# Performance work log

Hardware: AMD Instinct MI355X
Metric: run time of the kernel (lower is better)

## Reference

```python
import jax, jax.numpy as jnp
import numpy as np

D = 1024
H = 16
DH = D // H


def setup_inputs() -> dict:
    key = jax.random.key(0)
    ks = jax.random.split(key, 9)
    s = 1.0 / np.sqrt(D)
    x = jax.random.normal(ks[0], (4, 2048, D), dtype=jnp.float32)
    Wq = jax.random.uniform(ks[1], (D, D), jnp.float32, -s, s)
    bq = jax.random.uniform(ks[2], (D,), jnp.float32, -s, s)
    Wk = jax.random.uniform(ks[3], (D, D), jnp.float32, -s, s)
    bk = jax.random.uniform(ks[4], (D,), jnp.float32, -s, s)
    Wv = jax.random.uniform(ks[5], (D, D), jnp.float32, -s, s)
    bv = jax.random.uniform(ks[6], (D,), jnp.float32, -s, s)
    Wo = jax.random.uniform(ks[7], (D, D), jnp.float32, -s, s)
    bo = jax.random.uniform(ks[8], (D,), jnp.float32, -s, s)
    return {"x": x, "Wq": Wq, "bq": bq, "Wk": Wk, "bk": bk,
            "Wv": Wv, "bv": bv, "Wo": Wo, "bo": bo}


def _split_heads(t):
    b, s, d = t.shape
    return t.reshape(b, s, H, DH).transpose(0, 2, 1, 3)  # (B,H,S,Dh)


def reference(x, Wq, bq, Wk, bk, Wv, bv, Wo, bo):
    # Self-attention: context = x
    q = _split_heads(x @ Wq.T + bq)
    k = _split_heads(x @ Wk.T + bk)
    v = _split_heads(x @ Wv.T + bv)
    scale = 1.0 / np.sqrt(DH).astype(np.float32)
    logits = jnp.einsum('bhqd,bhkd->bhqk', q, k) * scale
    attn = jax.nn.softmax(logits, axis=-1)
    out_h = jnp.einsum('bhqk,bhkd->bhqd', attn, v)  # (B,H,S,Dh)
    b, h, s, dh = out_h.shape
    out = out_h.transpose(0, 2, 1, 3).reshape(b, s, h * dh)
    return out @ Wo.T + bo
```

## Files before the change

kernel.cpp:

```cpp
#include <hip/hip_runtime.h>
#include <cstdint>
#include <cstddef>

typedef unsigned short u16;
typedef __attribute__((ext_vector_type(8))) short short8;
typedef __attribute__((ext_vector_type(4))) short sv4;
typedef __attribute__((ext_vector_type(4))) float f32x4;
typedef __attribute__((ext_vector_type(2))) unsigned int u32x2;
typedef __attribute__((ext_vector_type(4))) unsigned int u32x4;

__device__ __forceinline__ u16 f2bf(float f) {
  unsigned int u = __builtin_bit_cast(unsigned int, f);
  u += 0x7FFFu + ((u >> 16) & 1u);
  return (u16)(u >> 16);
}
__device__ __forceinline__ float bf2f(u16 v) {
  return __builtin_bit_cast(float, ((unsigned int)v) << 16);
}

__device__ __forceinline__ unsigned int pk_bf16(float a, float b) {
#if defined(__HIP_DEVICE_COMPILE__) && __has_builtin(__builtin_amdgcn_cvt_pk_bf16_f32)
  typedef __attribute__((ext_vector_type(2))) __bf16 bf16x2;
  bf16x2 r = __builtin_amdgcn_cvt_pk_bf16_f32(a, b);
  return __builtin_bit_cast(unsigned int, r);
#else
  return (unsigned int)f2bf(a) | ((unsigned int)f2bf(b) << 16);
#endif
}

__device__ __forceinline__ f32x4 mfma_16x16x16_bf16(sv4 a, sv4 b, f32x4 c) {
#if defined(__HIP_DEVICE_COMPILE__)
#if __has_builtin(__builtin_amdgcn_mfma_f32_16x16x16bf16_1k)
  return __builtin_amdgcn_mfma_f32_16x16x16bf16_1k(a, b, c, 0, 0, 0);
#elif __has_builtin(__builtin_amdgcn_mfma_f32_16x16x16_bf16)
  return __builtin_amdgcn_mfma_f32_16x16x16_bf16(a, b, c, 0, 0, 0);
#else
  asm volatile("v_mfma_f32_16x16x16_bf16 %0, %1, %2, %0\n\ts_nop 7\n\ts_nop 4"
               : "+v"(c) : "v"(a), "v"(b));
  return c;
#endif
#else
  (void)a; (void)b;
  return c;
#endif
}

#define GLD_LDS(g, l) __builtin_amdgcn_global_load_lds( \
    (const __attribute__((address_space(1))) void*)(g), \
    (__attribute__((address_space(3))) void*)(l), 16, 0, 0)

#define QSCL 0.18033688011112042f

__global__ void detect_dtype(const u16* __restrict__ x, int* __restrict__ flag)
{
  const int lane = threadIdx.x;
  int hit = 0;
#pragma unroll
  for (int j = 0; j < 4; ++j) {
    float v = bf2f(x[lane * 4 + j]);
    if (!(v > -1000.f && v < 1000.f)) hit = 1;
  }
  unsigned long long any = __ballot(hit != 0);
  if (lane == 0) *flag = (any != 0ull) ? 1 : 0;
}

__global__ __launch_bounds__(256)
void convert_wb(const void* Wq, const void* Wk, const void* Wv, const void* Wo,
                const void* bq, const void* bk, const void* bv, const void* bo,
                u16* __restrict__ Wc, u16* __restrict__ bc, const int* __restrict__ flag)
{
  const int fp32 = *flag;
  const size_t base = ((size_t)blockIdx.x * 256 + threadIdx.x) * 8;
  const void* src; u16* dst; size_t local; int sel;
  if (base < (size_t)4 * 1048576) {
    sel = (int)(base >> 20);
    local = base & 1048575u;
    src = (sel == 0) ? Wq : (sel == 1) ? Wk : (sel == 2) ? Wv : Wo;
    dst = Wc + (size_t)sel * 1048576 + local;
  } else {
    const size_t rem = base - (size_t)4 * 1048576;
    sel = (int)(rem >> 10);
    local = rem & 1023u;
    src = (sel == 0) ? bq : (sel == 1) ? bk : (sel == 2) ? bv : bo;
    dst = bc + (size_t)sel * 1024 + local;
  }
  const float scale = (sel == 0) ? QSCL : 1.0f;
  if (fp32) {
    const float* s = (const float*)src + local;
    u32x4 w;
#pragma unroll
    for (int j = 0; j < 4; ++j) w[j] = pk_bf16(s[2 * j] * scale, s[2 * j + 1] * scale);
    *(short8*)dst = __builtin_bit_cast(short8, w);
  } else {
    const u16* s = (const u16*)src + local;
    if (sel == 0) {
      u32x4 w;
#pragma unroll
      for (int j = 0; j < 4; ++j)
        w[j] = pk_bf16(bf2f(s[2 * j]) * scale, bf2f(s[2 * j + 1]) * scale);
      *(short8*)dst = __builtin_bit_cast(short8, w);
    } else {
      *(short8*)dst = *(const short8*)s;
    }
  }
}

__global__ __launch_bounds__(256)
void convert_x_off(const void* __restrict__ x, u16* __restrict__ dst,
                   const int* __restrict__ flag, int b)
{
  const int fp32 = *flag;
  const size_t base = ((size_t)blockIdx.x * 256 + threadIdx.x) * 8;
  const size_t src_e = (size_t)b * 2048 * 1024 + base;
  if (fp32) {
    const float* s = (const float*)x + src_e;
    u32x4 w;
#pragma unroll
    for (int j = 0; j < 4; ++j) w[j] = pk_bf16(s[2 * j], s[2 * j + 1]);
    *(short8*)(dst + base) = __builtin_bit_cast(short8, w);
  } else {
    *(short8*)(dst + base) = *(const short8*)((const u16*)x + src_e);
  }
}

__global__ __launch_bounds__(256)
void gemm_bt(const u16* __restrict__ A,
             const u16* __restrict__ B0, const u16* __restrict__ B1, const u16* __restrict__ B2,
             const u16* __restrict__ bias, u16* __restrict__ C, int Ntot, int K)
{
  __shared__ __align__(16) u16 Alds[128 * 32];
  __shared__ __align__(16) u16 Blds[128 * 32];
  const int tid  = threadIdx.x;
  const int wave = tid >> 6, lane = tid & 63;
  const int quad = lane >> 4, l15 = lane & 15;
  const int m0  = blockIdx.x * 128;
  const int n0g = blockIdx.y * 128;
  const int sel = n0g >> 10;
  const u16* Bm = (sel == 0) ? B0 : ((sel == 1) ? B1 : B2);
  const u16* bb = bias + (size_t)sel * 1024;
  const int n0 = n0g & 1023;
  const int wr = (wave >> 1) * 64, wc = (wave & 1) * 64;

  f32x4 acc[4][4] = {};
  const int srow = lane >> 2;
  const int skc  = (lane & 3) * 8;
  const u16* Ag = A  + (size_t)(m0 + srow) * K + skc;
  const u16* Bg = Bm + (size_t)(n0 + srow) * K + skc;

  for (int kt = 0; kt < K; kt += 32) {
    __syncthreads();
#pragma unroll
    for (int t = 0; t < 2; ++t) {
      const int seg = wave * 2 + t;
      GLD_LDS(Ag + (size_t)(seg * 16) * K + kt, Alds + seg * 512);
      GLD_LDS(Bg + (size_t)(seg * 16) * K + kt, Blds + seg * 512);
    }
    __syncthreads();

    short8 af[4], bfr[4];
#pragma unroll
    for (int i = 0; i < 4; ++i)
      af[i] = *(const short8*)&Alds[(wr + i * 16 + l15) * 32 + quad * 8];
#pragma unroll
    for (int j = 0; j < 4; ++j)
      bfr[j] = *(const short8*)&Blds[(wc + j * 16 + l15) * 32 + quad * 8];
#pragma unroll
    for (int i = 0; i < 4; ++i)
#pragma unroll
      for (int j = 0; j < 4; ++j)
        acc[i][j] = __builtin_amdgcn_mfma_f32_16x16x32_bf16(af[i], bfr[j], acc[i][j], 0, 0, 0);
  }

#pragma unroll
  for (int i = 0; i < 4; ++i) {
    const int mr = m0 + wr + i * 16 + quad * 4;
#pragma unroll
    for (int j = 0; j < 4; ++j) {
      const int ncl = wc + j * 16 + l15;
      const float bvv = bf2f(bb[n0 + ncl]);
#pragma unroll
      for (int r = 0; r < 4; ++r)
        C[(size_t)(mr + r) * Ntot + n0g + ncl] = f2bf(acc[i][j][r] + bvv);
    }
  }
}

__global__ __launch_bounds__(256)
void gemm_bt_out(const u16* __restrict__ A, const u16* __restrict__ Bm,
                 const u16* __restrict__ bias, void* __restrict__ C16,
                 void* __restrict__ C32, int Ntot, int K, const int* __restrict__ flag)
{
  __shared__ __align__(16) u16 Alds[128 * 32];
  __shared__ __align__(16) u16 Blds[128 * 32];
  const int tid  = threadIdx.x;
  const int wave = tid >> 6, lane = tid & 63;
  const int quad = lane >> 4, l15 = lane & 15;
  const int m0 = blockIdx.x * 128;
  const int n0 = blockIdx.y * 128;
  const int wr = (wave >> 1) * 64, wc = (wave & 1) * 64;

  f32x4 acc[4][4] = {};
  const int srow = lane >> 2;
  const int skc  = (lane & 3) * 8;
  const u16* Ag = A  + (size_t)(m0 + srow) * K + skc;
  const u16* Bg = Bm + (size_t)(n0 + srow) * K + skc;

  for (int kt = 0; kt < K; kt += 32) {
    __syncthreads();
#pragma unroll
    for (int t = 0; t < 2; ++t) {
      const int seg = wave * 2 + t;
      GLD_LDS(Ag + (size_t)(seg * 16) * K + kt, Alds + seg * 512);
      GLD_LDS(Bg + (size_t)(seg * 16) * K + kt, Blds + seg * 512);
    }
    __syncthreads();

    short8 af[4], bfr[4];
#pragma unroll
    for (int i = 0; i < 4; ++i)
      af[i] = *(const short8*)&Alds[(wr + i * 16 + l15) * 32 + quad * 8];
#pragma unroll
    for (int j = 0; j < 4; ++j)
      bfr[j] = *(const short8*)&Blds[(wc + j * 16 + l15) * 32 + quad * 8];
#pragma unroll
    for (int i = 0; i < 4; ++i)
#pragma unroll
      for (int j = 0; j < 4; ++j)
        acc[i][j] = __builtin_amdgcn_mfma_f32_16x16x32_bf16(af[i], bfr[j], acc[i][j], 0, 0, 0);
  }

  if (*flag != 0) {
    float* Cf = (float*)C32;
#pragma unroll
    for (int i = 0; i < 4; ++i) {
      const int mr = m0 + wr + i * 16 + quad * 4;
#pragma unroll
      for (int j = 0; j < 4; ++j) {
        const int ncl = wc + j * 16 + l15;
        const float bvv = bf2f(bias[n0 + ncl]);
#pragma unroll
        for (int r = 0; r < 4; ++r)
          Cf[(size_t)(mr + r) * Ntot + n0 + ncl] = acc[i][j][r] + bvv;
      }
    }
  } else {
    u16* Cb = (u16*)C16;
#pragma unroll
    for (int i = 0; i < 4; ++i) {
      const int mr = m0 + wr + i * 16 + quad * 4;
#pragma unroll
      for (int j = 0; j < 4; ++j) {
        const int ncl = wc + j * 16 + l15;
        const float bvv = bf2f(bias[n0 + ncl]);
#pragma unroll
        for (int r = 0; r < 4; ++r)
          Cb[(size_t)(mr + r) * Ntot + n0 + ncl] = f2bf(acc[i][j][r] + bvv);
      }
    }
  }
}

__global__ __launch_bounds__(256, 4)
void attn_s(const u16* __restrict__ QKV, u16* __restrict__ O)
{
  __shared__ __align__(16) u16 Klds[64 * 72];
  __shared__ __align__(16) unsigned int Vlds[64 * 32];
  const int tid  = threadIdx.x;
  const int wave = tid >> 6, lane = tid & 63;
  const int quad = lane >> 4, l15 = lane & 15;
  const int qt = blockIdx.x, h = blockIdx.y;
  const u16* QKVb = QKV + (size_t)blockIdx.z * 2048 * 3072;
  u16* Ob = O + (size_t)blockIdx.z * 2048 * 1024;
  const int q0 = qt * 128;

  short8 qf[2][2];
  const u16* Qb = QKVb + (size_t)(q0 + wave * 32) * 3072 + h * 64;
#pragma unroll
  for (int rt = 0; rt < 2; ++rt)
#pragma unroll
    for (int kh = 0; kh < 2; ++kh)
      qf[rt][kh] = *(const short8*)(Qb + (size_t)(rt * 16 + l15) * 3072 + kh * 32 + quad * 8);

  f32x4 oaccT[4][2] = {};
  float lrow[2] = {};

  const int ksrow = tid >> 2;
  const int kscb  = (tid & 3) * 16;
  const int vkvp = lane & 31;
  const int vd0  = wave * 16 + (lane >> 5) * 8;

  const u16* Kb = QKVb + 1024 + h * 64;
  const u16* Vb = QKVb + 2048 + h * 64;

  for (int kv0 = 0; kv0 < 2048; kv0 += 64) {
    __syncthreads();
    {
      const u16* kp = Kb + (size_t)(kv0 + ksrow) * 3072 + kscb;
      *(short8*)&Klds[ksrow * 72 + kscb]     = *(const short8*)kp;
      *(short8*)&Klds[ksrow * 72 + kscb + 8] = *(const short8*)(kp + 8);

      const u16* v0p = Vb + (size_t)(kv0 + 2 * vkvp) * 3072 + vd0;
      short8 va = *(const short8*)v0p;
      short8 vb2 = *(const short8*)(v0p + 3072);
      const int kb = vkvp >> 1, kl = vkvp & 1;
#pragma unroll
      for (int j = 0; j < 8; ++j) {
        const int d = vd0 + j;
        Vlds[d * 32 + ((kb ^ (d & 15)) << 1) + kl] =
            ((unsigned int)(unsigned short)va[j]) |
            (((unsigned int)(unsigned short)vb2[j]) << 16);
      }
    }
    __syncthreads();

    f32x4 sacc[4][2] = {};
#pragma unroll
    for (int kh = 0; kh < 2; ++kh) {
      short8 kf[4];
#pragma unroll
      for (int ct = 0; ct < 4; ++ct)
        kf[ct] = *(const short8*)&Klds[(ct * 16 + l15) * 72 + kh * 32 + quad * 8];
#pragma unroll
      for (int ct = 0; ct < 4; ++ct)
#pragma unroll
        for (int rt = 0; rt < 2; ++rt)
          sacc[ct][rt] = __builtin_amdgcn_mfma_f32_16x16x32_bf16(kf[ct], qf[rt][kh], sacc[ct][rt], 0, 0, 0);
    }

    sv4 p16[4][2];
#pragma unroll
    for (int rt = 0; rt < 2; ++rt) {
      float rs = 0.f;
#pragma unroll
      for (int ct = 0; ct < 4; ++ct) {
        float p0 = __builtin_amdgcn_exp2f(sacc[ct][rt][0]);
        float p1 = __builtin_amdgcn_exp2f(sacc[ct][rt][1]);
        float p2 = __builtin_amdgcn_exp2f(sacc[ct][rt][2]);
        float p3 = __builtin_amdgcn_exp2f(sacc[ct][rt][3]);
        rs += (p0 + p1) + (p2 + p3);
        u32x2 pw;
        pw[0] = pk_bf16(p0, p1);
        pw[1] = pk_bf16(p2, p3);
        p16[ct][rt] = __builtin_bit_cast(sv4, pw);
      }
      rs += __shfl_xor(rs, 16, 64);
      rs += __shfl_xor(rs, 32, 64);
      lrow[rt] += rs;
    }

#pragma unroll
    for (int ct = 0; ct < 4; ++ct) {
#pragma unroll
      for (int dt = 0; dt < 4; ++dt) {
        const int d = dt * 16 + l15;
        const int idx = d * 32 + (((ct * 4 + quad) ^ (d & 15)) << 1);
        const sv4 vfr = *(const sv4*)&Vlds[idx];
#pragma unroll
        for (int rt = 0; rt < 2; ++rt)
          oaccT[dt][rt] = mfma_16x16x16_bf16(vfr, p16[ct][rt], oaccT[dt][rt]);
      }
    }
  }

#pragma unroll
  for (int rt = 0; rt < 2; ++rt) {
    const float inv = 1.f / lrow[rt];
    u16* Op = Ob + (size_t)(q0 + wave * 32 + rt * 16 + l15) * 1024 + h * 64;
#pragma unroll
    for (int dt = 0; dt < 4; ++dt) {
      u32x2 ow;
      ow[0] = pk_bf16(oaccT[dt][rt][0] * inv, oaccT[dt][rt][1] * inv);
      ow[1] = pk_bf16(oaccT[dt][rt][2] * inv, oaccT[dt][rt][3] * inv);
      *(sv4*)(Op + dt * 16 + quad * 4) = __builtin_bit_cast(sv4, ow);
    }
  }
}

extern "C" void kernel_launch(void* const* d_in, const int* in_sizes, int n_in,
                              void* d_out, int out_size, void* d_ws, size_t ws_size,
                              hipStream_t stream)
{
  int* flag = (int*)d_ws;
  u16* Wc   = (u16*)((char*)d_ws + 256);
  u16* bc   = Wc + (size_t)4 * 1048576;
  char* after_wb = (char*)(bc + 4096);

  detect_dtype<<<1, 64, 0, stream>>>((const u16*)d_in[0], flag);
  convert_wb<<<2050, 256, 0, stream>>>(d_in[1], d_in[3], d_in[5], d_in[7],
                                       d_in[2], d_in[4], d_in[6], d_in[8],
                                       Wc, bc, flag);

  const size_t need_batched =
      (size_t)(after_wb - (char*)d_ws) + ((size_t)8192 * 3072 + (size_t)8192 * 1024) * 2;

  if (ws_size >= need_batched) {
    u16* QKV = (u16*)after_wb;
    u16* xO  = QKV + (size_t)8192 * 3072;

    convert_x_off<<<4096, 256, 0, stream>>>(d_in[0], xO, flag, 0);
    gemm_bt<<<dim3(64, 24), 256, 0, stream>>>(xO, Wc, Wc + 1048576, Wc + 2097152,
                                              bc, QKV, 3072, 1024);
    attn_s<<<dim3(16, 16, 4), 256, 0, stream>>>(QKV, xO);
    gemm_bt_out<<<dim3(64, 8), 256, 0, stream>>>(xO, Wc + (size_t)3 * 1048576,
                                                 bc + 3 * 1024, d_out, d_out,
                                                 1024, 1024, flag);
  } else {
    u16* xc   = (u16*)after_wb;
    u16* QKVb = xc + (size_t)2048 * 1024;
    u16* Obb  = QKVb + (size_t)2048 * 3072;
    for (int b = 0; b < 4; ++b) {
      convert_x_off<<<1024, 256, 0, stream>>>(d_in[0], xc, flag, b);
      gemm_bt<<<dim3(16, 24), 256, 0, stream>>>(xc, Wc, Wc + 1048576, Wc + 2097152,
                                                bc, QKVb, 3072, 1024);
      attn_s<<<dim3(16, 16, 1), 256, 0, stream>>>(QKVb, Obb);
      void* outb16 = (void*)((char*)d_out + (size_t)b * 2048 * 1024 * 2);
      void* outb32 = (void*)((char*)d_out + (size_t)b * 2048 * 1024 * 4);
      gemm_bt_out<<<dim3(16, 8), 256, 0, stream>>>(Obb, Wc + (size_t)3 * 1048576,
                                                   bc + 3 * 1024, outb16, outb32,
                                                   1024, 1024, flag);
    }
  }
}
```

Measured before the change: 309.5 us.

## Double-buffer attention K/V tiles with direct global-to-LDS loads and transposed V reads

The attention kernel now stages K and V tiles with direct global-to-LDS loads (GLD_LDS) into two ping-pong LDS buffers, so the next tile's loads overlap the current tile's compute. K uses an XOR-swizzled layout in place of the padded one. The per-thread register repack of V into LDS is replaced by ds_read_b64_tr_b16 transposed reads. MFMA sections are wrapped in s_setprio. The cost is double the LDS footprint, which may lower occupancy, and more reliance on inline asm and exact waitcnt handling.

```diff
diff --git a/kernel.cpp b/kernel.cpp
--- a/kernel.cpp
+++ b/kernel.cpp
@@ -263,8 +263,8 @@
 __global__ __launch_bounds__(256, 4)
 void attn_s(const u16* __restrict__ QKV, u16* __restrict__ O)
 {
-  __shared__ __align__(16) u16 Klds[64 * 72];
-  __shared__ __align__(16) unsigned int Vlds[64 * 32];
+  __shared__ __align__(16) u16 Ka[64 * 64], Kb2[64 * 64];
+  __shared__ __align__(16) u16 Va[64 * 64], Vb2[64 * 64];
   const int tid  = threadIdx.x;
   const int wave = tid >> 6, lane = tid & 63;
   const int quad = lane >> 4, l15 = lane & 15;
@@ -284,47 +284,52 @@
   f32x4 oaccT[4][2] = {};
   float lrow[2] = {};
 
-  const int ksrow = tid >> 2;
-  const int kscb  = (tid & 3) * 16;
-  const int vkvp = lane & 31;
-  const int vd0  = wave * 16 + (lane >> 5) * 8;
-
-  const u16* Kb = QKVb + 1024 + h * 64;
-  const u16* Vb = QKVb + 2048 + h * 64;
-
-  for (int kv0 = 0; kv0 < 2048; kv0 += 64) {
-    __syncthreads();
-    {
-      const u16* kp = Kb + (size_t)(kv0 + ksrow) * 3072 + kscb;
-      *(short8*)&Klds[ksrow * 72 + kscb]     = *(const short8*)kp;
-      *(short8*)&Klds[ksrow * 72 + kscb + 8] = *(const short8*)(kp + 8);
-
-      const u16* v0p = Vb + (size_t)(kv0 + 2 * vkvp) * 3072 + vd0;
-      short8 va = *(const short8*)v0p;
-      short8 vb2 = *(const short8*)(v0p + 3072);
-      const int kb = vkvp >> 1, kl = vkvp & 1;
-#pragma unroll
-      for (int j = 0; j < 8; ++j) {
-        const int d = vd0 + j;
-        Vlds[d * 32 + ((kb ^ (d & 15)) << 1) + kl] =
-            ((unsigned int)(unsigned short)va[j]) |
-            (((unsigned int)(unsigned short)vb2[j]) << 16);
-      }
-    }
-    __syncthreads();
-
+  int koff[2][4];
+#pragma unroll
+  for (int kh = 0; kh < 2; ++kh)
+#pragma unroll
+    for (int ct = 0; ct < 4; ++ct) {
+      const int r = ct * 16 + l15;
+      koff[kh][ct] = r * 64 + (((kh * 4 + quad) ^ (r & 7)) << 3);
+    }
+
+  const u16* Kg = QKVb + 1024 + h * 64;
+  const u16* Vg = QKVb + 2048 + h * 64;
+  const u16* kg[2]; const u16* vg[2];
+#pragma unroll
+  for (int s = 0; s < 2; ++s) {
+    const int t = s * 256 + tid;
+    const int kvt = t >> 3, c = t & 7;
+    kg[s] = Kg + (size_t)kvt * 3072 + ((c ^ (kvt & 7)) << 3);
+    const int ct = t >> 7, dt = (t >> 5) & 3, kvl = (t >> 1) & 15, half = t & 1;
+    vg[s] = Vg + (size_t)(ct * 16 + kvl) * 3072 + dt * 16 + (half << 3);
+  }
+  const int ldsb = wave * 512;
+
+  auto stage = [&](u16* KL, u16* VL) {
+    GLD_LDS(kg[0], KL + ldsb);
+    GLD_LDS(kg[1], KL + 2048 + ldsb);
+    GLD_LDS(vg[0], VL + ldsb);
+    GLD_LDS(vg[1], VL + 2048 + ldsb);
+    kg[0] += 64 * 3072; kg[1] += 64 * 3072;
+    vg[0] += 64 * 3072; vg[1] += 64 * 3072;
+  };
+
+  auto tile = [&](const u16* KL, const u16* VL) {
     f32x4 sacc[4][2] = {};
 #pragma unroll
     for (int kh = 0; kh < 2; ++kh) {
       short8 kf[4];
 #pragma unroll
       for (int ct = 0; ct < 4; ++ct)
-        kf[ct] = *(const short8*)&Klds[(ct * 16 + l15) * 72 + kh * 32 + quad * 8];
+        kf[ct] = *(const short8*)&KL[koff[kh][ct]];
+      __builtin_amdgcn_s_setprio(1);
 #pragma unroll
       for (int ct = 0; ct < 4; ++ct)
 #pragma unroll
         for (int rt = 0; rt < 2; ++rt)
           sacc[ct][rt] = __builtin_amdgcn_mfma_f32_16x16x32_bf16(kf[ct], qf[rt][kh], sacc[ct][rt], 0, 0, 0);
+      __builtin_amdgcn_s_setprio(0);
     }
 
     sv4 p16[4][2];
@@ -350,16 +355,34 @@
 
 #pragma unroll
     for (int ct = 0; ct < 4; ++ct) {
+      sv4 vfr[4];
 #pragma unroll
       for (int dt = 0; dt < 4; ++dt) {
-        const int d = dt * 16 + l15;
-        const int idx = d * 32 + (((ct * 4 + quad) ^ (d & 15)) << 1);
-        const sv4 vfr = *(const sv4*)&Vlds[idx];
+        const __attribute__((address_space(3))) u16* vp =
+            (const __attribute__((address_space(3))) u16*)&VL[ct * 1024 + dt * 256 + lane * 4];
+        asm volatile("ds_read_b64_tr_b16 %0, %1" : "=v"(vfr[dt]) : "v"(vp));
+      }
+      asm volatile("s_waitcnt lgkmcnt(0)" ::: "memory");
+      __builtin_amdgcn_sched_barrier(0);
+      __builtin_amdgcn_s_setprio(1);
+#pragma unroll
+      for (int dt = 0; dt < 4; ++dt)
 #pragma unroll
         for (int rt = 0; rt < 2; ++rt)
-          oaccT[dt][rt] = mfma_16x16x16_bf16(vfr, p16[ct][rt], oaccT[dt][rt]);
-      }
-    }
+          oaccT[dt][rt] = mfma_16x16x16_bf16(vfr[dt], p16[ct][rt], oaccT[dt][rt]);
+      __builtin_amdgcn_s_setprio(0);
+    }
+  };
+
+  stage(Ka, Va);
+#pragma unroll 1
+  for (int it = 0; it < 16; ++it) {
+    __syncthreads();
+    stage(Kb2, Vb2);
+    tile(Ka, Va);
+    __syncthreads();
+    if (it != 15) stage(Ka, Va);
+    tile(Kb2, Vb2);
   }
 
 #pragma unroll
```

Measured after the change: 449.2 us. 1.45x slower.

## Double-buffer K/V tiles with direct global-to-LDS loads and transposed V reads

Applied to the files above, without the earlier changes.

Rewrites the attention inner loop to ping-pong between two LDS buffers for K and V. The next tile is loaded straight from global into LDS while the current tile is computed. V is stored untransposed and read with ds_read_b64_tr_b16 instead of being transposed through registers, and the K layout moves to an XOR swizzle without padding. MFMA sections are wrapped in s_setprio to favour matrix issue. The aim is to hide global load latency and drop the register-side transpose work, at the cost of more LDS use, which may limit occupancy.

```diff
diff --git a/kernel.cpp b/kernel.cpp
--- a/kernel.cpp
+++ b/kernel.cpp
@@ -260,11 +260,80 @@
   }
 }
 
+
+#define STAGE(KL, VL) do {                         \
+    GLD_LDS(kg0, (KL) + ldsb);                     \
+    GLD_LDS(kg1, (KL) + 2048 + ldsb);              \
+    GLD_LDS(vg0, (VL) + ldsb);                     \
+    GLD_LDS(vg1, (VL) + 2048 + ldsb);              \
+    kg0 += ADV; kg1 += ADV; vg0 += ADV; vg1 += ADV;\
+  } while (0)
+
+#define ATILE(KL, VL) do {                                                     \
+    f32x4 sacc[4][2] = {};                                                     \
+    _Pragma("unroll")                                                          \
+    for (int kh = 0; kh < 2; ++kh) {                                           \
+      const int kof = kh ? koff1 : koff0;                                      \
+      short8 kf[4];                                                            \
+      _Pragma("unroll")                                                        \
+      for (int ct = 0; ct < 4; ++ct)                                           \
+        kf[ct] = *(const short8*)&(KL)[ct * 1024 + kof];                       \
+      __builtin_amdgcn_s_setprio(1);                                           \
+      _Pragma("unroll")                                                        \
+      for (int ct = 0; ct < 4; ++ct)                                           \
+        _Pragma("unroll")                                                      \
+        for (int rt = 0; rt < 2; ++rt)                                         \
+          sacc[ct][rt] = __builtin_amdgcn_mfma_f32_16x16x32_bf16(              \
+              kf[ct], qf[rt][kh], sacc[ct][rt], 0, 0, 0);                      \
+      __builtin_amdgcn_s_setprio(0);                                           \
+    }                                                                          \
+    sv4 p16[4][2];                                                             \
+    _Pragma("unroll")                                                          \
+    for (int rt = 0; rt < 2; ++rt) {                                           \
+      float rs = 0.f;                                                          \
+      _Pragma("unroll")                                                        \
+      for (int ct = 0; ct < 4; ++ct) {                                         \
+        float p0 = __builtin_amdgcn_exp2f(sacc[ct][rt][0]);                    \
+        float p1 = __builtin_amdgcn_exp2f(sacc[ct][rt][1]);                    \
+        float p2 = __builtin_amdgcn_exp2f(sacc[ct][rt][2]);                    \
+        float p3 = __builtin_amdgcn_exp2f(sacc[ct][rt][3]);                    \
+        rs += (p0 + p1) + (p2 + p3);                                           \
+        u32x2 pw;                                                              \
+        pw[0] = pk_bf16(p0, p1);                                               \
+        pw[1] = pk_bf16(p2, p3);                                               \
+        p16[ct][rt] = __builtin_bit_cast(sv4, pw);                             \
+      }                                                                        \
+      rs += __shfl_xor(rs, 16, 64);                                            \
+      rs += __shfl_xor(rs, 32, 64);                                            \
+      lrow[rt] += rs;                                                          \
+    }                                                                          \
+    const __attribute__((address_space(3))) u16* vpb =                         \
+        (const __attribute__((address_space(3))) u16*)(VL) + lane * 4;         \
+    _Pragma("unroll")                                                          \
+    for (int ct = 0; ct < 4; ++ct) {                                           \
+      sv4 vfr[4];                                                              \
+      _Pragma("unroll")                                                        \
+      for (int dt = 0; dt < 4; ++dt)                                           \
+        asm volatile("ds_read_b64_tr_b16 %0, %1"                               \
+                     : "=v"(vfr[dt]) : "v"(vpb + ct * 1024 + dt * 256));       \
+      asm volatile("s_waitcnt lgkmcnt(0)" ::: "memory");                       \
+      __builtin_amdgcn_sched_barrier(0);                         \
+      __builtin_amdgcn_s_setprio(1);                                           \
+      _Pragma("unroll")                                                        \
+      for (int dt = 0; dt < 4; ++dt)                                           \
+        _Pragma("unroll")                                                      \
+        for (int rt = 0; rt < 2; ++rt)                                         \
+          oaccT[dt][rt] = mfma_16x16x16_bf16(vfr[dt], p16[ct][rt],             \
+                                             oaccT[dt][rt]);                   \
+      __builtin_amdgcn_s_setprio(0);                                           \
+    }                                                                          \
+  } while (0)
+
 __global__ __launch_bounds__(256, 4)
 void attn_s(const u16* __restrict__ QKV, u16* __restrict__ O)
 {
-  __shared__ __align__(16) u16 Klds[64 * 72];
-  __shared__ __align__(16) unsigned int Vlds[64 * 32];
+  __shared__ __align__(16) u16 Ka[64 * 64], Kb[64 * 64];
+  __shared__ __align__(16) u16 Va[64 * 64], Vb[64 * 64];
   const int tid  = threadIdx.x;
   const int wave = tid >> 6, lane = tid & 63;
   const int quad = lane >> 4, l15 = lane & 15;
@@ -284,82 +353,30 @@
   f32x4 oaccT[4][2] = {};
   float lrow[2] = {};
 
-  const int ksrow = tid >> 2;
-  const int kscb  = (tid & 3) * 16;
-  const int vkvp = lane & 31;
-  const int vd0  = wave * 16 + (lane >> 5) * 8;
-
-  const u16* Kb = QKVb + 1024 + h * 64;
-  const u16* Vb = QKVb + 2048 + h * 64;
-
-  for (int kv0 = 0; kv0 < 2048; kv0 += 64) {
-    __syncthreads();
-    {
-      const u16* kp = Kb + (size_t)(kv0 + ksrow) * 3072 + kscb;
-      *(short8*)&Klds[ksrow * 72 + kscb]     = *(const short8*)kp;
-      *(short8*)&Klds[ksrow * 72 + kscb + 8] = *(const short8*)(kp + 8);
-
-      const u16* v0p = Vb + (size_t)(kv0 + 2 * vkvp) * 3072 + vd0;
-      short8 va = *(const short8*)v0p;
-      short8 vb2 = *(const short8*)(v0p + 3072);
-      const int kb = vkvp >> 1, kl = vkvp & 1;
-#pragma unroll
-      for (int j = 0; j < 8; ++j) {
-        const int d = vd0 + j;
-        Vlds[d * 32 + ((kb ^ (d & 15)) << 1) + kl] =
-            ((unsigned int)(unsigned short)va[j]) |
-            (((unsigned int)(unsigned short)vb2[j]) << 16);
-      }
-    }
-    __syncthreads();
-
-    f32x4 sacc[4][2] = {};
-#pragma unroll
-    for (int kh = 0; kh < 2; ++kh) {
-      short8 kf[4];
-#pragma unroll
-      for (int ct = 0; ct < 4; ++ct)
-        kf[ct] = *(const short8*)&Klds[(ct * 16 + l15) * 72 + kh * 32 + quad * 8];
-#pragma unroll
-      for (int ct = 0; ct < 4; ++ct)
-#pragma unroll
-        for (int rt = 0; rt < 2; ++rt)
-          sacc[ct][rt] = __builtin_amdgcn_mfma_f32_16x16x32_bf16(kf[ct], qf[rt][kh], sacc[ct][rt], 0, 0, 0);
-    }
-
-    sv4 p16[4][2];
-#pragma unroll
-    for (int rt = 0; rt < 2; ++rt) {
-      float rs = 0.f;
-#pragma unroll
-      for (int ct = 0; ct < 4; ++ct) {
-        float p0 = __builtin_amdgcn_exp2f(sacc[ct][rt][0]);
-        float p1 = __builtin_amdgcn_exp2f(sacc[ct][rt][1]);
-        float p2 = __builtin_amdgcn_exp2f(sacc[ct][rt][2]);
-        float p3 = __builtin_amdgcn_exp2f(sacc[ct][rt][3]);
-        rs += (p0 + p1) + (p2 + p3);
-        u32x2 pw;
-        pw[0] = pk_bf16(p0, p1);
-        pw[1] = pk_bf16(p2, p3);
-        p16[ct][rt] = __builtin_bit_cast(sv4, pw);
-      }
-      rs += __shfl_xor(rs, 16, 64);
-      rs += __shfl_xor(rs, 32, 64);
-      lrow[rt] += rs;
-    }
-
-#pragma unroll
-    for (int ct = 0; ct < 4; ++ct) {
-#pragma unroll
-      for (int dt = 0; dt < 4; ++dt) {
-        const int d = dt * 16 + l15;
-        const int idx = d * 32 + (((ct * 4 + quad) ^ (d & 15)) << 1);
-        const sv4 vfr = *(const sv4*)&Vlds[idx];
-#pragma unroll
-        for (int rt = 0; rt < 2; ++rt)
-          oaccT[dt][rt] = mfma_16x16x16_bf16(vfr, p16[ct][rt], oaccT[dt][rt]);
-      }
-    }
+  const int koff0 = l15 * 64 + ((quad       ^ (l15 & 7)) << 3);
+  const int koff1 = l15 * 64 + (((4 + quad) ^ (l15 & 7)) << 3);
+
+  const u16* Kg = QKVb + 1024 + h * 64;
+  const u16* Vg = QKVb + 2048 + h * 64;
+  const int t0 = tid, t1 = 256 + tid;
+  const u16* kg0 = Kg + (size_t)(t0 >> 3) * 3072 + (((t0 & 7) ^ ((t0 >> 3) & 7)) << 3);
+  const u16* kg1 = Kg + (size_t)(t1 >> 3) * 3072 + (((t1 & 7) ^ ((t1 >> 3) & 7)) << 3);
+  const u16* vg0 = Vg + (size_t)((t0 >> 7) * 16 + ((t0 >> 1) & 15)) * 3072
+                      + ((t0 >> 5) & 3) * 16 + ((t0 & 1) << 3);
+  const u16* vg1 = Vg + (size_t)((t1 >> 7) * 16 + ((t1 >> 1) & 15)) * 3072
+                      + ((t1 >> 5) & 3) * 16 + ((t1 & 1) << 3);
+  const int ldsb = wave * 512;
+  const size_t ADV = (size_t)64 * 3072;
+
+  STAGE(Ka, Va);
+#pragma unroll 1
+  for (int it = 0; it < 16; ++it) {
+    __syncthreads();
+    STAGE(Kb, Vb);
+    ATILE(Ka, Va);
+    __syncthreads();
+    if (it != 15) STAGE(Ka, Va);
+    ATILE(Kb, Vb);
   }
 
 #pragma unroll
```

Measured after the change: 444.6 us. 43.7% more time.

## Enlarge attention blocks to 256 queries with swizzled grid and MFMA priority

Applied to the files above, without the earlier changes.

The attention kernel now runs 512-thread blocks of 8 waves, each covering 256 query rows. Each K/V tile staged in shared memory is therefore reused by twice as many queries, which halves global K/V traffic and the load work per query. A 1D grid with a remapped block index groups blocks for the same batch and nearby heads so K/V stays in L2, and s_setprio raises wave priority around the MFMA sections. Only half the threads do the tile loads, and the larger blocks lower the number of resident blocks and the parallelism per CU.

```diff
diff --git a/kernel.cpp b/kernel.cpp
--- a/kernel.cpp
+++ b/kernel.cpp
@@ -260,7 +260,7 @@
   }
 }
 
-__global__ __launch_bounds__(256, 4)
+__global__ __launch_bounds__(512, 4)
 void attn_s(const u16* __restrict__ QKV, u16* __restrict__ O)
 {
   __shared__ __align__(16) u16 Klds[64 * 72];
@@ -268,10 +268,17 @@
   const int tid  = threadIdx.x;
   const int wave = tid >> 6, lane = tid & 63;
   const int quad = lane >> 4, l15 = lane & 15;
-  const int qt = blockIdx.x, h = blockIdx.y;
-  const u16* QKVb = QKV + (size_t)blockIdx.z * 2048 * 3072;
-  u16* Ob = O + (size_t)blockIdx.z * 2048 * 1024;
-  const int q0 = qt * 128;
+
+  const int i  = blockIdx.x;
+  const int j  = i >> 3;
+  const int qt = j & 7;
+  const int g  = (i & 7) + ((j >> 3) << 3);
+  const int h  = g & 15;
+  const int z  = g >> 4;
+
+  const u16* QKVb = QKV + (size_t)z * 2048 * 3072;
+  u16* Ob = O + (size_t)z * 2048 * 1024;
+  const int q0 = qt * 256;
 
   short8 qf[2][2];
   const u16* Qb = QKVb + (size_t)(q0 + wave * 32) * 3072 + h * 64;
@@ -289,26 +296,26 @@
   const int vkvp = lane & 31;
   const int vd0  = wave * 16 + (lane >> 5) * 8;
 
-  const u16* Kb = QKVb + 1024 + h * 64;
-  const u16* Vb = QKVb + 2048 + h * 64;
+  const u16* Kg = QKVb + 1024 + h * 64;
+  const u16* Vg = QKVb + 2048 + h * 64;
 
   for (int kv0 = 0; kv0 < 2048; kv0 += 64) {
     __syncthreads();
-    {
-      const u16* kp = Kb + (size_t)(kv0 + ksrow) * 3072 + kscb;
+    if (tid < 256) {
+      const u16* kp = Kg + (size_t)(kv0 + ksrow) * 3072 + kscb;
       *(short8*)&Klds[ksrow * 72 + kscb]     = *(const short8*)kp;
       *(short8*)&Klds[ksrow * 72 + kscb + 8] = *(const short8*)(kp + 8);
 
-      const u16* v0p = Vb + (size_t)(kv0 + 2 * vkvp) * 3072 + vd0;
-      short8 va = *(const short8*)v0p;
+      const u16* v0p = Vg + (size_t)(kv0 + 2 * vkvp) * 3072 + vd0;
+      short8 va  = *(const short8*)v0p;
       short8 vb2 = *(const short8*)(v0p + 3072);
       const int kb = vkvp >> 1, kl = vkvp & 1;
 #pragma unroll
-      for (int j = 0; j < 8; ++j) {
-        const int d = vd0 + j;
+      for (int jj = 0; jj < 8; ++jj) {
+        const int d = vd0 + jj;
         Vlds[d * 32 + ((kb ^ (d & 15)) << 1) + kl] =
-            ((unsigned int)(unsigned short)va[j]) |
-            (((unsigned int)(unsigned short)vb2[j]) << 16);
+            ((unsigned int)(unsigned short)va[jj]) |
+            (((unsigned int)(unsigned short)vb2[jj]) << 16);
       }
     }
     __syncthreads();
@@ -320,11 +327,13 @@
 #pragma unroll
       for (int ct = 0; ct < 4; ++ct)
         kf[ct] = *(const short8*)&Klds[(ct * 16 + l15) * 72 + kh * 32 + quad * 8];
+      __builtin_amdgcn_s_setprio(1);
 #pragma unroll
       for (int ct = 0; ct < 4; ++ct)
 #pragma unroll
         for (int rt = 0; rt < 2; ++rt)
           sacc[ct][rt] = __builtin_amdgcn_mfma_f32_16x16x32_bf16(kf[ct], qf[rt][kh], sacc[ct][rt], 0, 0, 0);
+      __builtin_amdgcn_s_setprio(0);
     }
 
     sv4 p16[4][2];
@@ -348,6 +357,7 @@
       lrow[rt] += rs;
     }
 
+    __builtin_amdgcn_s_setprio(1);
 #pragma unroll
     for (int ct = 0; ct < 4; ++ct) {
 #pragma unroll
@@ -360,6 +370,7 @@
           oaccT[dt][rt] = mfma_16x16x16_bf16(vfr, p16[ct][rt], oaccT[dt][rt]);
       }
     }
+    __builtin_amdgcn_s_setprio(0);
   }
 
 #pragma unroll
@@ -400,7 +411,7 @@
     convert_x_off<<<4096, 256, 0, stream>>>(d_in[0], xO, flag, 0);
     gemm_bt<<<dim3(64, 24), 256, 0, stream>>>(xO, Wc, Wc + 1048576, Wc + 2097152,
                                               bc, QKV, 3072, 1024);
-    attn_s<<<dim3(16, 16, 4), 256, 0, stream>>>(QKV, xO);
+    attn_s<<<512, 512, 0, stream>>>(QKV, xO);
     gemm_bt_out<<<dim3(64, 8), 256, 0, stream>>>(xO, Wc + (size_t)3 * 1048576,
                                                  bc + 3 * 1024, d_out, d_out,
                                                  1024, 1024, flag);
@@ -412,7 +423,7 @@
       convert_x_off<<<1024, 256, 0, stream>>>(d_in[0], xc, flag, b);
       gemm_bt<<<dim3(16, 24), 256, 0, stream>>>(xc, Wc, Wc + 1048576, Wc + 2097152,
                                                 bc, QKVb, 3072, 1024);
-      attn_s<<<dim3(16, 16, 1), 256, 0, stream>>>(QKVb, Obb);
+      attn_s<<<128, 512, 0, stream>>>(QKVb, Obb);
       void* outb16 = (void*)((char*)d_out + (size_t)b * 2048 * 1024 * 2);
       void* outb32 = (void*)((char*)d_out + (size_t)b * 2048 * 1024 * 4);
       gemm_bt_out<<<dim3(16, 8), 256, 0, stream>>>(Obb, Wc + (size_t)3 * 1048576,
```

Result: no change. 308.5 us (-0.3%).
